# Optimization experiments

Measured on AMD Instinct MI355X. Metric: run time of the kernel, lower is better.

Reference implementation:

```python
import jax, jax.numpy as jnp
import numpy as np

B, N, DIM = 8, 4096, 1024
H, DH = 16, 64          # heads, dim_head -> inner_dim = 1024
P = 256                 # proj_size (Linformer low-rank seq projection)
SCALE = DH ** -0.5


def setup_inputs() -> dict:
    key = jax.random.key(0)
    ks = jax.random.split(key, 6)
    return {
        "x": jax.random.normal(ks[0], (B, N, DIM), dtype=jnp.float32),
        "Wqkv": jax.random.normal(ks[1], (3 * H * DH, DIM), dtype=jnp.float32) * 0.02,
        "We": jax.random.normal(ks[2], (P, N), dtype=jnp.float32) * 0.02,
        "be": jax.random.normal(ks[3], (P,), dtype=jnp.float32) * 0.02,
        "Wo": jax.random.normal(ks[4], (DIM, H * DH), dtype=jnp.float32) * 0.02,
        "bo": jax.random.normal(ks[5], (DIM,), dtype=jnp.float32) * 0.02,
    }


def reference(x, Wqkv, We, be, Wo, bo):
    b, n, _ = x.shape
    # fused QKV projection (no bias), split, reshape to (b, h, n, d)
    qkv = jnp.einsum('bnc,ec->bne', x, Wqkv)                      # [b, n, 3*h*d]
    q, k, v = jnp.split(qkv, 3, axis=-1)
    tohead = lambda t: t.reshape(b, n, H, DH).transpose(0, 2, 1, 3)
    q, k, v = tohead(q), tohead(k), tohead(v)
    # shared E=F sequence projection: Linear over seq axis n -> p, bias along p
    kp = jnp.einsum('bhnd,pn->bhpd', k, We) + be[None, None, :, None]
    vp = jnp.einsum('bhnd,pn->bhpd', v, We) + be[None, None, :, None]
    dots = jnp.einsum('bhid,bhjd->bhij', q, kp) * SCALE           # [b, h, n, p]
    attn = jax.nn.softmax(dots, axis=-1)
    out = jnp.einsum('bhij,bhjd->bhid', attn, vp)                 # [b, h, n, d]
    out = out.transpose(0, 2, 1, 3).reshape(b, n, H * DH)
    return jnp.einsum('bne,oe->bno', out, Wo) + bo                # [b, n, dim]
```

## Files before the change

kernel.cpp:

```cpp
#include <hip/hip_runtime.h>
#include <hip/hip_bf16.h>


typedef unsigned short bf16u;
typedef __attribute__((ext_vector_type(8))) short short8;
typedef __attribute__((ext_vector_type(4))) float f32x4;

__device__ __forceinline__ unsigned short f2bf(float f) {
    unsigned u = __float_as_uint(f);
    u += 0x7FFF + ((u >> 16) & 1);
    return (unsigned short)(u >> 16);
}

__device__ __forceinline__ f32x4 mfma16(short8 a, short8 b, f32x4 c) {
    return __builtin_amdgcn_mfma_f32_16x16x32_bf16(a, b, c, 0, 0, 0);
}

#define AS1 __attribute__((address_space(1)))
#define AS3 __attribute__((address_space(3)))

__global__ void cvt_kernel(const float* __restrict__ in, bf16u* __restrict__ out, int n4) {
    int i = blockIdx.x * blockDim.x + threadIdx.x;
    int stride = gridDim.x * blockDim.x;
    for (int j = i; j < n4; j += stride) {
        float4 v = ((const float4*)in)[j];
        union { bf16u s[4]; uint2 u; } o;
        o.s[0] = f2bf(v.x); o.s[1] = f2bf(v.y); o.s[2] = f2bf(v.z); o.s[3] = f2bf(v.w);
        ((uint2*)out)[j] = o.u;
    }
}

__global__ __launch_bounds__(256) void cvt_transpose_x(const float* __restrict__ x,
                                                       bf16u* __restrict__ Xbf,
                                                       bf16u* __restrict__ XT) {
    __shared__ bf16u T[64][72];
    const int b = blockIdx.z;
    const int n0 = blockIdx.y * 64, c0 = blockIdx.x * 64;
    const int t = threadIdx.x;
    const int cx = t & 15, ry = t >> 4;
#pragma unroll
    for (int p = 0; p < 4; p++) {
        const int nn = p * 16 + ry;
        const size_t g = ((size_t)b * 4096 + n0 + nn) * 1024 + c0 + cx * 4;
        float4 v = *(const float4*)&x[g];
        union { bf16u s[4]; uint2 u; } o;
        o.s[0] = f2bf(v.x); o.s[1] = f2bf(v.y); o.s[2] = f2bf(v.z); o.s[3] = f2bf(v.w);
        *(uint2*)&Xbf[g] = o.u;
#pragma unroll
        for (int j = 0; j < 4; j++) T[cx * 4 + j][nn] = o.s[j];
    }
    __syncthreads();
    const int cc = t >> 2, ch = t & 3;
#pragma unroll
    for (int j = 0; j < 2; j++) {
        const int nch = ch + j * 4;
        short8 vv = *(const short8*)&T[cc][nch * 8];
        *(short8*)&XT[((size_t)b * 1024 + c0 + cc) * 4096 + n0 + nch * 8] = vv;
    }
}

__device__ __forceinline__ void gemm_core_128(const bf16u* __restrict__ Ablk, int ldA,
                                              const bf16u* __restrict__ Bblk, int ldB,
                                              int Kiter, f32x4 (&acc)[4][4]) {
    __shared__ __align__(16) bf16u As[128 * 32];
    __shared__ __align__(16) bf16u Bs[128 * 32];
    const int t = threadIdx.x;
    const int wave = t >> 6, lane = t & 63;
    const int wm = (wave >> 1) * 64, wn = (wave & 1) * 64;
    const int lr = lane & 15, lk = (lane >> 4) * 8;

    for (int kt = 0; kt < Kiter; kt += 32) {
#pragma unroll
        for (int i = 0; i < 2; i++) {
            int c = i * 256 + wave * 64 + lane;
            const bf16u* ga = Ablk + (size_t)(c >> 2) * ldA + kt + (c & 3) * 8;
            const bf16u* gb = Bblk + (size_t)(c >> 2) * ldB + kt + (c & 3) * 8;
            __builtin_amdgcn_global_load_lds((const AS1 unsigned*)ga,
                (AS3 unsigned*)(&As[(i * 256 + wave * 64) * 8]), 16, 0, 0);
            __builtin_amdgcn_global_load_lds((const AS1 unsigned*)gb,
                (AS3 unsigned*)(&Bs[(i * 256 + wave * 64) * 8]), 16, 0, 0);
        }
        __syncthreads();
        short8 a[4], b[4];
#pragma unroll
        for (int mi = 0; mi < 4; mi++)
            a[mi] = *(const short8*)&As[(wm + mi * 16 + lr) * 32 + lk];
#pragma unroll
        for (int ni = 0; ni < 4; ni++)
            b[ni] = *(const short8*)&Bs[(wn + ni * 16 + lr) * 32 + lk];
#pragma unroll
        for (int mi = 0; mi < 4; mi++)
#pragma unroll
            for (int ni = 0; ni < 4; ni++)
                acc[mi][ni] = mfma16(a[mi], b[ni], acc[mi][ni]);
        __syncthreads();
    }
}

__global__ __launch_bounds__(256) void gemm_ex_splitk(const bf16u* __restrict__ We,
                                                      const bf16u* __restrict__ XT,
                                                      float* __restrict__ Cpart) {
    const int bn = blockIdx.x, bm = blockIdx.y;
    const int bz = blockIdx.z >> 2, ks = blockIdx.z & 3;
    f32x4 acc[4][4];
#pragma unroll
    for (int i = 0; i < 4; i++)
#pragma unroll
        for (int j = 0; j < 4; j++) acc[i][j] = f32x4{0.f, 0.f, 0.f, 0.f};

    gemm_core_128(We + (size_t)bm * 128 * 4096 + ks * 1024, 4096,
                  XT + ((size_t)bz * 1024 + bn * 128) * 4096 + ks * 1024, 4096,
                  1024, acc);

    const int lane = threadIdx.x & 63, wave = threadIdx.x >> 6;
    const int wm = (wave >> 1) * 64, wn = (wave & 1) * 64;
    const int lr = lane & 15, lg = (lane >> 4) * 4;
    float* Cp = Cpart + (size_t)(ks * 8 + bz) * 256 * 1024;
#pragma unroll
    for (int ni = 0; ni < 4; ni++) {
        const int col = bn * 128 + wn + ni * 16 + lr;
#pragma unroll
        for (int mi = 0; mi < 4; mi++) {
#pragma unroll
            for (int r = 0; r < 4; r++) {
                const int row = bm * 128 + wm + mi * 16 + lg + r;
                Cp[(size_t)row * 1024 + col] = acc[mi][ni][r];
            }
        }
    }
}

__global__ __launch_bounds__(256) void reduce4_cvt(const float* __restrict__ P,
                                                   bf16u* __restrict__ out) {
    const int j = blockIdx.x * blockDim.x + threadIdx.x;
    const float4* p = (const float4*)P;
    float4 s0 = p[j], s1 = p[j + 524288], s2 = p[j + 1048576], s3 = p[j + 1572864];
    union { bf16u s[4]; uint2 u; } o;
    o.s[0] = f2bf((s0.x + s1.x) + (s2.x + s3.x));
    o.s[1] = f2bf((s0.y + s1.y) + (s2.y + s3.y));
    o.s[2] = f2bf((s0.z + s1.z) + (s2.z + s3.z));
    o.s[3] = f2bf((s0.w + s1.w) + (s2.w + s3.w));
    ((uint2*)out)[j] = o.u;
}

__global__ __launch_bounds__(256) void gemm_kpv(const bf16u* __restrict__ EX,
                                                const bf16u* __restrict__ Wkv,
                                                const float* __restrict__ be,
                                                bf16u* __restrict__ kp,
                                                bf16u* __restrict__ vpT) {
    const int bn = blockIdx.x, bm = blockIdx.y, bz = blockIdx.z;
    f32x4 acc[4][4];
#pragma unroll
    for (int i = 0; i < 4; i++)
#pragma unroll
        for (int j = 0; j < 4; j++) acc[i][j] = f32x4{0.f, 0.f, 0.f, 0.f};

    gemm_core_128(EX + (size_t)bz * 256 * 1024 + (size_t)bm * 128 * 1024, 1024,
                  Wkv + (size_t)bn * 128 * 1024, 1024, 1024, acc);

    const int lane = threadIdx.x & 63, wave = threadIdx.x >> 6;
    const int wm = (wave >> 1) * 64, wn = (wave & 1) * 64;
    const int lr = lane & 15, lg = (lane >> 4) * 4;
    bf16u* kpB = kp + (size_t)bz * 256 * 1024;
    bf16u* vpB = vpT + (size_t)bz * 1024 * 256;
    const int ebase = bn * 128 + wn;
#pragma unroll
    for (int ni = 0; ni < 4; ni++) {
        const int col = ebase + ni * 16 + lr;
        const int region = (ebase + ni * 16) >> 10;
#pragma unroll
        for (int mi = 0; mi < 4; mi++) {
            const int p0 = bm * 128 + wm + mi * 16 + lg;
            if (region == 0) {
#pragma unroll
                for (int r = 0; r < 4; r++)
                    kpB[(size_t)(p0 + r) * 1024 + col] = f2bf(acc[mi][ni][r] + be[p0 + r]);
            } else {
                const int d = col - 1024;
                union { bf16u s[4]; uint2 u; } o;
#pragma unroll
                for (int r = 0; r < 4; r++) o.s[r] = f2bf(acc[mi][ni][r] + be[p0 + r]);
                *(uint2*)&vpB[(size_t)d * 256 + p0] = o.u;
            }
        }
    }
}

template<int MODE>
__global__ __launch_bounds__(512, 2) void gemm_deep(const bf16u* __restrict__ A,
                                                    const bf16u* __restrict__ Bt,
                                                    const float* __restrict__ bias,
                                                    void* __restrict__ Cout,
                                                    int K) {
    __shared__ __align__(16) bf16u L[3 * 24576];

    const int nwg = gridDim.x;
    const int bid = blockIdx.x;
    const int logical = (bid & 7) * (nwg >> 3) + (bid >> 3);
    const int bn = logical & 7, bm = logical >> 3;

    const bf16u* Ablk = A + (size_t)bm * 256 * K;
    const bf16u* Bblk = Bt + (size_t)bn * 128 * K;

    const int t = threadIdx.x;
    const int wid = t >> 6, lane = t & 63;
    const int wm = (wid >> 1) * 64, wn = (wid & 1) * 64;
    const int lr = lane & 15, g4 = lane >> 4;

    f32x4 acc[4][4];
#pragma unroll
    for (int i = 0; i < 4; i++)
#pragma unroll
        for (int j = 0; j < 4; j++) acc[i][j] = f32x4{0.f, 0.f, 0.f, 0.f};

    auto STAGE_A = [&](int buf, int kt, int half) {
#pragma unroll
        for (int i = 0; i < 2; i++) {
            const int c = half * 1024 + i * 512 + t;
            const int row = c >> 3, gp = c & 7;
            const int col = kt * 64 + ((gp ^ (row & 7)) << 3);
            __builtin_amdgcn_global_load_lds(
                (const AS1 unsigned*)(Ablk + (size_t)row * K + col),
                (AS3 unsigned*)(&L[buf * 24576 + c * 8]), 16, 0, 0);
        }
    };
    auto STAGE_B = [&](int buf, int kt) {
#pragma unroll
        for (int i = 0; i < 2; i++) {
            const int c = i * 512 + t;
            const int row = c >> 3, gp = c & 7;
            const int col = kt * 64 + ((gp ^ (row & 7)) << 3);
            __builtin_amdgcn_global_load_lds(
                (const AS1 unsigned*)(Bblk + (size_t)row * K + col),
                (AS3 unsigned*)(&L[buf * 24576 + 16384 + c * 8]), 16, 0, 0);
        }
    };

    short8 aF[2][2], bF[4][2];
    auto LDA = [&](int buf, int msub) {
#pragma unroll
        for (int mi = 0; mi < 2; mi++) {
            const int R = wm + msub * 32 + mi * 16 + lr;
#pragma unroll
            for (int ks = 0; ks < 2; ks++) {
                const int gp = (ks * 4 + g4) ^ (R & 7);
                aF[mi][ks] = *(const short8*)&L[buf * 24576 + R * 64 + gp * 8];
            }
        }
    };
    auto LDB = [&](int buf, int nsub) {
#pragma unroll
        for (int ni = 0; ni < 2; ni++) {
            const int R = wn + nsub * 32 + ni * 16 + lr;
#pragma unroll
            for (int ks = 0; ks < 2; ks++) {
                const int gp = (ks * 4 + g4) ^ (R & 7);
                bF[nsub * 2 + ni][ks] = *(const short8*)&L[buf * 24576 + 16384 + R * 64 + gp * 8];
            }
        }
    };
    auto MM = [&](int msub, int nsub) {
        __builtin_amdgcn_s_setprio(1);
#pragma unroll
        for (int mi = 0; mi < 2; mi++)
#pragma unroll
            for (int nj = 0; nj < 2; nj++)
#pragma unroll
                for (int ks = 0; ks < 2; ks++)
                    acc[msub * 2 + mi][nsub * 2 + nj] =
                        mfma16(aF[mi][ks], bF[nsub * 2 + nj][ks], acc[msub * 2 + mi][nsub * 2 + nj]);
        __builtin_amdgcn_s_setprio(0);
    };
    auto BAR = [&]() {
        asm volatile("" ::: "memory");
        __builtin_amdgcn_s_barrier();
        asm volatile("" ::: "memory");
    };
    auto WAIT_LGKM0 = [&]() {
        asm volatile("s_waitcnt lgkmcnt(0)" ::: "memory");
        __builtin_amdgcn_sched_barrier(0);
    };

    const int nkt = K >> 6;

    STAGE_A(0, 0, 0); STAGE_A(0, 0, 1); STAGE_B(0, 0);
    STAGE_A(1, 1, 0); STAGE_A(1, 1, 1); STAGE_B(1, 1);
    asm volatile("s_waitcnt vmcnt(6)" ::: "memory");
    BAR();

    int cur = 0;
    for (int j = 0; j < nkt; j++) {
        const bool stg = (j + 2 < nkt);
        const int sbuf = (cur >= 1) ? cur - 1 : 2;

        LDA(cur, 0); LDB(cur, 0);
        if (stg) STAGE_A(sbuf, j + 2, 0);
        BAR(); WAIT_LGKM0();
        MM(0, 0);
        BAR();
        LDB(cur, 1);
        if (stg) STAGE_A(sbuf, j + 2, 1);
        BAR(); WAIT_LGKM0();
        MM(0, 1);
        BAR();
        LDA(cur, 1);
        if (stg) STAGE_B(sbuf, j + 2);
        BAR(); WAIT_LGKM0();
        MM(1, 1);
        BAR();
        MM(1, 0);
        if (j < nkt - 2) asm volatile("s_waitcnt vmcnt(6)" ::: "memory");
        else             asm volatile("s_waitcnt vmcnt(0)" ::: "memory");
        BAR();

        cur = (cur == 2) ? 0 : cur + 1;
    }

    const int lg = g4 * 4;
    if (MODE == 0) {
        bf16u* C = (bf16u*)Cout;
#pragma unroll
        for (int mi = 0; mi < 4; mi++) {
#pragma unroll
            for (int r = 0; r < 4; r++) {
                const size_t row = (size_t)bm * 256 + wm + mi * 16 + lg + r;
#pragma unroll
                for (int ni = 0; ni < 4; ni++)
                    C[row * 1024 + bn * 128 + wn + ni * 16 + lr] = f2bf(acc[mi][ni][r]);
            }
        }
    } else {
        float* C = (float*)Cout;
        float bv[4];
#pragma unroll
        for (int ni = 0; ni < 4; ni++) bv[ni] = bias[bn * 128 + wn + ni * 16 + lr];
#pragma unroll
        for (int mi = 0; mi < 4; mi++) {
#pragma unroll
            for (int r = 0; r < 4; r++) {
                const size_t row = (size_t)bm * 256 + wm + mi * 16 + lg + r;
#pragma unroll
                for (int ni = 0; ni < 4; ni++)
                    C[row * 1024 + bn * 128 + wn + ni * 16 + lr] = acc[mi][ni][r] + bv[ni];
            }
        }
    }
}

__global__ __launch_bounds__(256, 2) void attn_kernel(const bf16u* __restrict__ Q,
                                                      const bf16u* __restrict__ kp,
                                                      const bf16u* __restrict__ vpT,
                                                      bf16u* __restrict__ O) {
    __shared__ __align__(16) bf16u S[32768];
    const int bh = blockIdx.y, b = bh >> 4, h = bh & 15;
    const int t = threadIdx.x;
    const int wave = t >> 6, lane = t & 63;
    const int lr = lane & 15, g = lane >> 4;
    const int i0 = blockIdx.x * 64 + wave * 16;
    const size_t mrow = (size_t)b * 4096 + i0;

    short8 bq[2];
    const bf16u* Qb = Q + (mrow + lr) * 1024 + h * 64 + g * 8;
    bq[0] = *(const short8*)&Qb[0];
    bq[1] = *(const short8*)&Qb[32];

    const bf16u* kpb = kp + ((size_t)b * 256) * 1024 + h * 64;
    const bf16u* vpb = vpT + ((size_t)b * 1024 + h * 64) * 256;
#pragma unroll
    for (int i = 0; i < 8; i++) {
        const int c = i * 256 + t;
        const int ubase = (i * 256 + wave * 64) * 8;
        {
            const int p = c >> 3, d8 = (c & 7) ^ (p & 7);
            __builtin_amdgcn_global_load_lds(
                (const AS1 unsigned*)(kpb + (size_t)p * 1024 + d8 * 8),
                (AS3 unsigned*)&S[ubase], 16, 0, 0);
        }
        {
            const int d = c >> 5, p8 = (c & 31) ^ (d & 15);
            __builtin_amdgcn_global_load_lds(
                (const AS1 unsigned*)(vpb + (size_t)d * 256 + p8 * 8),
                (AS3 unsigned*)&S[16384 + ubase], 16, 0, 0);
        }
    }
    __syncthreads();

    f32x4 dots[16];
#pragma unroll
    for (int pj = 0; pj < 16; pj++) dots[pj] = f32x4{0.f, 0.f, 0.f, 0.f};
#pragma unroll
    for (int pj = 0; pj < 16; pj++) {
#pragma unroll
        for (int kk = 0; kk < 2; kk++) {
            const int gr = (pj * 16 + lr) * 8 + ((kk * 4 + g) ^ (lr & 7));
            short8 ak = *(const short8*)&S[gr * 8];
            dots[pj] = mfma16(ak, bq[kk], dots[pj]);
        }
    }

    float s = 0.f;
#pragma unroll
    for (int pj = 0; pj < 16; pj++) {
#pragma unroll
        for (int r = 0; r < 4; r++) {
            float e = __expf(dots[pj][r] * 0.125f);
            dots[pj][r] = e;
            s += e;
        }
    }
    s += __shfl_xor(s, 16);
    s += __shfl_xor(s, 32);
    const float inv = 1.0f / s;

    __syncthreads();

    const int pbase = wave * 4096 + lr * 256;
    const int pxor = (lr & 7) << 3;
#pragma unroll
    for (int pj = 0; pj < 16; pj++) {
        unsigned lo = (unsigned)f2bf(dots[pj][0] * inv) | ((unsigned)f2bf(dots[pj][1] * inv) << 16);
        unsigned hi = (unsigned)f2bf(dots[pj][2] * inv) | ((unsigned)f2bf(dots[pj][3] * inv) << 16);
        const int el = (pbase + pj * 16 + g * 4) ^ pxor;
        uint2 u; u.x = lo; u.y = hi;
        *(uint2*)&S[el] = u;
    }

    f32x4 oacc[4];
#pragma unroll
    for (int dj = 0; dj < 4; dj++) oacc[dj] = f32x4{0.f, 0.f, 0.f, 0.f};
#pragma unroll
    for (int pk = 0; pk < 8; pk++) {
        const int el = (pbase + pk * 32 + g * 8) ^ pxor;
        short8 ap = *(const short8*)&S[el];
#pragma unroll
        for (int dj = 0; dj < 4; dj++) {
            const int d = dj * 16 + lr;
            const int gr = d * 32 + ((pk * 4 + g) ^ (d & 15));
            short8 bv = *(const short8*)&S[16384 + gr * 8];
            oacc[dj] = mfma16(ap, bv, oacc[dj]);
        }
    }

    bf16u* Ob = O + (mrow + g * 4) * 1024 + h * 64 + lr;
#pragma unroll
    for (int dj = 0; dj < 4; dj++)
#pragma unroll
        for (int r = 0; r < 4; r++)
            Ob[(size_t)r * 1024 + dj * 16] = f2bf(oacc[dj][r]);
}

extern "C" void kernel_launch(void* const* d_in, const int* in_sizes, int n_in,
                              void* d_out, int out_size, void* d_ws, size_t ws_size,
                              hipStream_t stream) {
    const float* x    = (const float*)d_in[0];
    const float* Wqkv = (const float*)d_in[1];
    const float* We   = (const float*)d_in[2];
    const float* be   = (const float*)d_in[3];
    const float* Wo   = (const float*)d_in[4];
    const float* bo   = (const float*)d_in[5];
    float* out = (float*)d_out;

    char* w = (char*)d_ws;
    bf16u* Qbf  = (bf16u*)(w);
    bf16u* Obuf = (bf16u*)(w + 67108864ull);
    bf16u* Wqb  = (bf16u*)(w + 134217728ull);
    bf16u* Web  = (bf16u*)(w + 140509184ull);
    bf16u* Wob  = (bf16u*)(w + 142606336ull);
    bf16u* EXb  = (bf16u*)(w + 144703488ull);
    if (ws_size < 148897792ull) return;

    bf16u* Xbf = (bf16u*)d_out;
    bf16u* XT  = Xbf + 33554432ull;
    float* EXpart = (float*)d_out;
    bf16u* kpb = Xbf;
    bf16u* vpb = Xbf + 2097152ull;

    cvt_transpose_x<<<dim3(16, 64, 8), 256, 0, stream>>>(x, Xbf, XT);
    cvt_kernel<<<768, 256, 0, stream>>>(Wqkv, Wqb, 3145728 / 4);
    cvt_kernel<<<256, 256, 0, stream>>>(We,   Web, 1048576 / 4);
    cvt_kernel<<<256, 256, 0, stream>>>(Wo,   Wob, 1048576 / 4);

    gemm_deep<0><<<1024, 512, 0, stream>>>(Xbf, Wqb, nullptr, Qbf, 1024);
    gemm_ex_splitk<<<dim3(8, 2, 32), 256, 0, stream>>>(Web, XT, EXpart);
    reduce4_cvt<<<2048, 256, 0, stream>>>(EXpart, EXb);
    gemm_kpv<<<dim3(16, 2, 8), 256, 0, stream>>>(EXb, Wqb + (size_t)1024 * 1024, be, kpb, vpb);

    attn_kernel<<<dim3(64, 128), 256, 0, stream>>>(Qbf, kpb, vpb, Obuf);
    gemm_deep<1><<<1024, 512, 0, stream>>>(Obuf, Wob, bo, out, 1024);
}
```

Before: 374.7 us.

## Enlarge GEMM tile to 256x256 with 8-wave ping-pong double buffering

```diff
diff --git a/kernel.cpp b/kernel.cpp
--- a/kernel.cpp
+++ b/kernel.cpp
@@ -187,88 +187,78 @@
 }
 
 template<int MODE>
-__global__ __launch_bounds__(512, 2) void gemm_deep(const bf16u* __restrict__ A,
-                                                    const bf16u* __restrict__ Bt,
-                                                    const float* __restrict__ bias,
-                                                    void* __restrict__ Cout,
-                                                    int K) {
-    __shared__ __align__(16) bf16u L[3 * 24576];
+__global__ __launch_bounds__(512, 2) void gemm8p(const bf16u* __restrict__ A,
+                                                 const bf16u* __restrict__ Bt,
+                                                 const float* __restrict__ bias,
+                                                 void* __restrict__ Cout,
+                                                 int K) {
+    __shared__ __align__(16) bf16u L[2][32768];
 
     const int nwg = gridDim.x;
     const int bid = blockIdx.x;
     const int logical = (bid & 7) * (nwg >> 3) + (bid >> 3);
-    const int bn = logical & 7, bm = logical >> 3;
+    const int bn = logical & 3, bm = logical >> 2;
 
     const bf16u* Ablk = A + (size_t)bm * 256 * K;
-    const bf16u* Bblk = Bt + (size_t)bn * 128 * K;
+    const bf16u* Bblk = Bt + (size_t)bn * 256 * K;
 
     const int t = threadIdx.x;
     const int wid = t >> 6, lane = t & 63;
-    const int wm = (wid >> 1) * 64, wn = (wid & 1) * 64;
+    const int wm = (wid >> 2) * 128, wn = (wid & 3) * 64;
     const int lr = lane & 15, g4 = lane >> 4;
 
-    f32x4 acc[4][4];
-#pragma unroll
-    for (int i = 0; i < 4; i++)
+    f32x4 acc[8][4];
+#pragma unroll
+    for (int i = 0; i < 8; i++)
 #pragma unroll
         for (int j = 0; j < 4; j++) acc[i][j] = f32x4{0.f, 0.f, 0.f, 0.f};
 
-    auto STAGE_A = [&](int buf, int kt, int half) {
-#pragma unroll
-        for (int i = 0; i < 2; i++) {
-            const int c = half * 1024 + i * 512 + t;
-            const int row = c >> 3, gp = c & 7;
-            const int col = kt * 64 + ((gp ^ (row & 7)) << 3);
-            __builtin_amdgcn_global_load_lds(
-                (const AS1 unsigned*)(Ablk + (size_t)row * K + col),
-                (AS3 unsigned*)(&L[buf * 24576 + c * 8]), 16, 0, 0);
-        }
-    };
-    auto STAGE_B = [&](int buf, int kt) {
+    auto STAGE = [&](int buf, int which, int half, int kt) {
 #pragma unroll
         for (int i = 0; i < 2; i++) {
             const int c = i * 512 + t;
-            const int row = c >> 3, gp = c & 7;
+            const int row = half * 128 + (c >> 3);
+            const int gp = c & 7;
             const int col = kt * 64 + ((gp ^ (row & 7)) << 3);
-            __builtin_amdgcn_global_load_lds(
-                (const AS1 unsigned*)(Bblk + (size_t)row * K + col),
-                (AS3 unsigned*)(&L[buf * 24576 + 16384 + c * 8]), 16, 0, 0);
+            const bf16u* src = (which ? Bblk : Ablk) + (size_t)row * K + col;
+            __builtin_amdgcn_global_load_lds((const AS1 unsigned*)src,
+                (AS3 unsigned*)(&L[buf][which * 16384 + half * 8192 + c * 8]), 16, 0, 0);
         }
     };
 
-    short8 aF[2][2], bF[4][2];
-    auto LDA = [&](int buf, int msub) {
-#pragma unroll
-        for (int mi = 0; mi < 2; mi++) {
-            const int R = wm + msub * 32 + mi * 16 + lr;
+    short8 aF[4][2], bE[2][2], bO[2][2];
+    auto LDA = [&](int buf, int mq) {
+#pragma unroll
+        for (int mi = 0; mi < 4; mi++) {
+            const int row = wm + mq * 64 + mi * 16 + lr;
 #pragma unroll
             for (int ks = 0; ks < 2; ks++) {
-                const int gp = (ks * 4 + g4) ^ (R & 7);
-                aF[mi][ks] = *(const short8*)&L[buf * 24576 + R * 64 + gp * 8];
+                const int gp = (ks * 4 + g4) ^ (row & 7);
+                aF[mi][ks] = *(const short8*)&L[buf][row * 64 + gp * 8];
             }
         }
     };
-    auto LDB = [&](int buf, int nsub) {
+    auto LDB = [&](int buf, int nq, short8 (&bF)[2][2]) {
 #pragma unroll
         for (int ni = 0; ni < 2; ni++) {
-            const int R = wn + nsub * 32 + ni * 16 + lr;
+            const int row = wn + nq * 32 + ni * 16 + lr;
 #pragma unroll
             for (int ks = 0; ks < 2; ks++) {
-                const int gp = (ks * 4 + g4) ^ (R & 7);
-                bF[nsub * 2 + ni][ks] = *(const short8*)&L[buf * 24576 + 16384 + R * 64 + gp * 8];
+                const int gp = (ks * 4 + g4) ^ (row & 7);
+                bF[ni][ks] = *(const short8*)&L[buf][16384 + row * 64 + gp * 8];
             }
         }
     };
-    auto MM = [&](int msub, int nsub) {
+    auto MM = [&](int mq, int nq, short8 (&bF)[2][2]) {
         __builtin_amdgcn_s_setprio(1);
 #pragma unroll
-        for (int mi = 0; mi < 2; mi++)
+        for (int mi = 0; mi < 4; mi++)
 #pragma unroll
             for (int nj = 0; nj < 2; nj++)
 #pragma unroll
                 for (int ks = 0; ks < 2; ks++)
-                    acc[msub * 2 + mi][nsub * 2 + nj] =
-                        mfma16(aF[mi][ks], bF[nsub * 2 + nj][ks], acc[msub * 2 + mi][nsub * 2 + nj]);
+                    acc[mq * 4 + mi][nq * 2 + nj] =
+                        mfma16(aF[mi][ks], bF[nj][ks], acc[mq * 4 + mi][nq * 2 + nj]);
         __builtin_amdgcn_s_setprio(0);
     };
     auto BAR = [&]() {
@@ -276,72 +266,94 @@
         __builtin_amdgcn_s_barrier();
         asm volatile("" ::: "memory");
     };
-    auto WAIT_LGKM0 = [&]() {
+    auto LGKM0 = [&]() {
         asm volatile("s_waitcnt lgkmcnt(0)" ::: "memory");
         __builtin_amdgcn_sched_barrier(0);
     };
 
     const int nkt = K >> 6;
-
-    STAGE_A(0, 0, 0); STAGE_A(0, 0, 1); STAGE_B(0, 0);
-    STAGE_A(1, 1, 0); STAGE_A(1, 1, 1); STAGE_B(1, 1);
-    asm volatile("s_waitcnt vmcnt(6)" ::: "memory");
+    const int niter = nkt >> 1;
+
+    STAGE(0, 0, 0, 0); STAGE(0, 0, 1, 0); STAGE(0, 1, 0, 0); STAGE(0, 1, 1, 0);
+    STAGE(1, 0, 0, 1); STAGE(1, 0, 1, 1); STAGE(1, 1, 0, 1); STAGE(1, 1, 1, 1);
+    asm volatile("s_waitcnt vmcnt(8)" ::: "memory");
     BAR();
 
-    int cur = 0;
-    for (int j = 0; j < nkt; j++) {
-        const bool stg = (j + 2 < nkt);
-        const int sbuf = (cur >= 1) ? cur - 1 : 2;
-
-        LDA(cur, 0); LDB(cur, 0);
-        if (stg) STAGE_A(sbuf, j + 2, 0);
-        BAR(); WAIT_LGKM0();
-        MM(0, 0);
-        BAR();
-        LDB(cur, 1);
-        if (stg) STAGE_A(sbuf, j + 2, 1);
-        BAR(); WAIT_LGKM0();
-        MM(0, 1);
-        BAR();
-        LDA(cur, 1);
-        if (stg) STAGE_B(sbuf, j + 2);
-        BAR(); WAIT_LGKM0();
-        MM(1, 1);
-        BAR();
-        MM(1, 0);
-        if (j < nkt - 2) asm volatile("s_waitcnt vmcnt(6)" ::: "memory");
-        else             asm volatile("s_waitcnt vmcnt(0)" ::: "memory");
-        BAR();
-
-        cur = (cur == 2) ? 0 : cur + 1;
+    for (int it = 0; it < niter; it++) {
+        const int kt1 = 2 * it + 1, kt2 = 2 * it + 2, kt3 = 2 * it + 3;
+        const bool p123 = (it > 0), s4 = (kt2 < nkt), s8 = (kt3 < nkt);
+
+        LDA(0, 0); LDB(0, 0, bE);
+        if (p123) STAGE(1, 0, 1, kt1);
+        asm volatile("s_waitcnt lgkmcnt(8)" ::: "memory");
+        BAR(); LGKM0();
+        MM(0, 0, bE);
+        BAR();
+        LDB(0, 1, bO);
+        if (p123) STAGE(1, 1, 0, kt1);
+        BAR(); LGKM0();
+        MM(0, 1, bO);
+        BAR();
+        LDA(0, 1);
+        if (p123) STAGE(1, 1, 1, kt1);
+        BAR(); LGKM0();
+        MM(1, 1, bO);
+        BAR();
+        if (s4) STAGE(0, 0, 0, kt2);
+        MM(1, 0, bE);
+        if (s4) asm volatile("s_waitcnt vmcnt(2)" ::: "memory");
+        else    asm volatile("s_waitcnt vmcnt(0)" ::: "memory");
+        BAR();
+
+        LDA(1, 0); LDB(1, 0, bE);
+        if (s4) STAGE(0, 0, 1, kt2);
+        asm volatile("s_waitcnt lgkmcnt(8)" ::: "memory");
+        BAR(); LGKM0();
+        MM(0, 0, bE);
+        BAR();
+        LDB(1, 1, bO);
+        if (s4) STAGE(0, 1, 0, kt2);
+        BAR(); LGKM0();
+        MM(0, 1, bO);
+        BAR();
+        LDA(1, 1);
+        if (s4) STAGE(0, 1, 1, kt2);
+        BAR(); LGKM0();
+        MM(1, 1, bO);
+        BAR();
+        if (s8) STAGE(1, 0, 0, kt3);
+        MM(1, 0, bE);
+        if (s8) asm volatile("s_waitcnt vmcnt(2)" ::: "memory");
+        else    asm volatile("s_waitcnt vmcnt(0)" ::: "memory");
+        BAR();
     }
 
     const int lg = g4 * 4;
     if (MODE == 0) {
         bf16u* C = (bf16u*)Cout;
 #pragma unroll
-        for (int mi = 0; mi < 4; mi++) {
+        for (int mi = 0; mi < 8; mi++) {
 #pragma unroll
             for (int r = 0; r < 4; r++) {
                 const size_t row = (size_t)bm * 256 + wm + mi * 16 + lg + r;
 #pragma unroll
                 for (int ni = 0; ni < 4; ni++)
-                    C[row * 1024 + bn * 128 + wn + ni * 16 + lr] = f2bf(acc[mi][ni][r]);
+                    C[row * 1024 + bn * 256 + wn + ni * 16 + lr] = f2bf(acc[mi][ni][r]);
             }
         }
     } else {
         float* C = (float*)Cout;
         float bv[4];
 #pragma unroll
-        for (int ni = 0; ni < 4; ni++) bv[ni] = bias[bn * 128 + wn + ni * 16 + lr];
-#pragma unroll
-        for (int mi = 0; mi < 4; mi++) {
+        for (int ni = 0; ni < 4; ni++) bv[ni] = bias[bn * 256 + wn + ni * 16 + lr];
+#pragma unroll
+        for (int mi = 0; mi < 8; mi++) {
 #pragma unroll
             for (int r = 0; r < 4; r++) {
                 const size_t row = (size_t)bm * 256 + wm + mi * 16 + lg + r;
 #pragma unroll
                 for (int ni = 0; ni < 4; ni++)
-                    C[row * 1024 + bn * 128 + wn + ni * 16 + lr] = acc[mi][ni][r] + bv[ni];
+                    C[row * 1024 + bn * 256 + wn + ni * 16 + lr] = acc[mi][ni][r] + bv[ni];
             }
         }
     }
@@ -480,11 +492,11 @@
     cvt_kernel<<<256, 256, 0, stream>>>(We,   Web, 1048576 / 4);
     cvt_kernel<<<256, 256, 0, stream>>>(Wo,   Wob, 1048576 / 4);
 
-    gemm_deep<0><<<1024, 512, 0, stream>>>(Xbf, Wqb, nullptr, Qbf, 1024);
+    gemm8p<0><<<512, 512, 0, stream>>>(Xbf, Wqb, nullptr, Qbf, 1024);
     gemm_ex_splitk<<<dim3(8, 2, 32), 256, 0, stream>>>(Web, XT, EXpart);
     reduce4_cvt<<<2048, 256, 0, stream>>>(EXpart, EXb);
     gemm_kpv<<<dim3(16, 2, 8), 256, 0, stream>>>(EXb, Wqb + (size_t)1024 * 1024, be, kpb, vpb);
 
     attn_kernel<<<dim3(64, 128), 256, 0, stream>>>(Qbf, kpb, vpb, Obuf);
-    gemm_deep<1><<<1024, 512, 0, stream>>>(Obuf, Wob, bo, out, 1024);
-}
+    gemm8p<1><<<512, 512, 0, stream>>>(Obuf, Wob, bo, out, 1024);
+}
```

Result: faster. 364.4 us (-2.8%).
